# Optimization experiments

Hardware: AMD Instinct MI355X
Metric: run time of the kernel (lower is better)

## Reference

```python
import jax, jax.numpy as jnp
import numpy as np

EMBED_DIM = 2048
NUM_HEADS = 32
NUM_KV_HEADS = 8
HEAD_DIM = EMBED_DIM // NUM_HEADS  # 64
KV_DIM = HEAD_DIM * NUM_KV_HEADS   # 512
ROPE_BASE = 10000.0


def rope_cos_sin(seq_len, dim):
    inv_freq = 1.0 / (ROPE_BASE ** (jnp.arange(0, dim, 2, dtype=jnp.float32) / dim))
    t = jnp.arange(seq_len, dtype=jnp.float32)
    freqs = jnp.outer(t, inv_freq)                 # [T, dim/2]
    emb = jnp.concatenate([freqs, freqs], axis=-1)  # [T, dim]
    return jnp.cos(emb), jnp.sin(emb)


def rotate_half(x):
    half = x.shape[-1] // 2
    return jnp.concatenate([-x[..., half:], x[..., :half]], axis=-1)


def setup_inputs() -> dict:
    key = jax.random.key(0)
    k_x, k_q, k_k, k_v, k_o = jax.random.split(key, 5)
    B, T, C = 2, 2048, EMBED_DIM
    s = 1.0 / np.sqrt(C)
    x = jax.random.normal(k_x, (B, T, C), dtype=jnp.float32)
    # Linear weights stored as [in, out]; no bias (bias=False)
    Wq = jax.random.normal(k_q, (C, EMBED_DIM), dtype=jnp.float32) * s
    Wk = jax.random.normal(k_k, (C, KV_DIM), dtype=jnp.float32) * s
    Wv = jax.random.normal(k_v, (C, KV_DIM), dtype=jnp.float32) * s
    Wo = jax.random.normal(k_o, (C, EMBED_DIM), dtype=jnp.float32) * s
    return {"x": x, "Wq": Wq, "Wk": Wk, "Wv": Wv, "Wo": Wo}


def reference(x, Wq, Wk, Wv, Wo):
    B, T, C = x.shape
    H, KVH, D = NUM_HEADS, NUM_KV_HEADS, HEAD_DIM
    scale = D ** -0.5
    rep = H // KVH

    q = (x @ Wq).reshape(B, T, H, D).transpose(0, 2, 1, 3)    # [B,H,T,D]
    k = (x @ Wk).reshape(B, T, KVH, D).transpose(0, 2, 1, 3)  # [B,KVH,T,D]
    v = (x @ Wv).reshape(B, T, KVH, D).transpose(0, 2, 1, 3)
    # repeat_interleave over head dim to expand KV heads
    k = jnp.repeat(k, rep, axis=1)  # [B,H,T,D]
    v = jnp.repeat(v, rep, axis=1)

    cos, sin = rope_cos_sin(T, D)
    cos = cos[None, None, :, :]
    sin = sin[None, None, :, :]
    q = q * cos + rotate_half(q) * sin
    k = k * cos + rotate_half(k) * sin

    att = jnp.einsum('bhtd,bhsd->bhts', q, k) * scale  # [B,H,T,T]
    att = jax.nn.softmax(att, axis=-1)                 # mask=None, dropout eval
    y = jnp.einsum('bhts,bhsd->bhtd', att, v)          # [B,H,T,D]
    y = y.transpose(0, 2, 1, 3).reshape(B, T, C)
    return y @ Wo
```

## Files before the change

### kernel.cpp

```cpp
#include <hip/hip_runtime.h>
#include <stdint.h>

#define Tn   2048
#define Cn   2048
#define Hn   32
#define KVHn 8
#define Dn   64
#define MR   4096
#define NQKV 3072
#define KD   2048

typedef __attribute__((ext_vector_type(4))) float fx4;
typedef __attribute__((ext_vector_type(8))) short frag8;

#define MFMA(a,b,c) __builtin_amdgcn_mfma_f32_16x16x32_bf16((a),(b),(c),0,0,0)

struct __align__(16) U16x8 { unsigned short s[8]; };

__device__ __forceinline__ unsigned short f2bf(float x){
  union { float f; unsigned u; } v; v.f = x;
  return (unsigned short)((v.u + 0x7FFFu + ((v.u >> 16) & 1u)) >> 16);
}
__device__ __forceinline__ float bf2f(unsigned short h){
  union { unsigned u; float f; } v; v.u = ((unsigned)h) << 16; return v.f;
}
__device__ __forceinline__ float sexp2(float x){
#if __has_builtin(__builtin_amdgcn_exp2f)
  return __builtin_amdgcn_exp2f(x);
#else
  return exp2f(x);
#endif
}
__device__ __forceinline__ unsigned cvtpk(float a, float b){
  unsigned r; asm("v_cvt_pk_bf16_f32 %0, %1, %2" : "=v"(r) : "v"(a), "v"(b)); return r;
}

typedef const __attribute__((address_space(1))) void cas1_void;
typedef __attribute__((address_space(3))) void as3_void;
__device__ __forceinline__ void gld16(const void* g, void* l){
  __builtin_amdgcn_global_load_lds((cas1_void*)g, (as3_void*)l, 16, 0, 0);
}

__global__ __launch_bounds__(256) void k_prep(const float* __restrict__ x, unsigned short* __restrict__ xb,
                                              const float* __restrict__ Wq, const float* __restrict__ Wk,
                                              const float* __restrict__ Wv, unsigned short* __restrict__ wqkvt,
                                              const float* __restrict__ Wo, unsigned short* __restrict__ wot,
                                              float2* __restrict__ cs){
  __shared__ float tile[64][65];
  int blk = blockIdx.x, t = threadIdx.x;
  if (blk < 2048) {
    size_t blockbase = (size_t)blk * 4096;
    #pragma unroll
    for (int j = 0; j < 4; ++j) {
      size_t i = blockbase + j * 1024 + t * 4;
      float4 v = *(const float4*)(x + i);
      ushort4 o; o.x = f2bf(v.x); o.y = f2bf(v.y); o.z = f2bf(v.z); o.w = f2bf(v.w);
      *(ushort4*)(xb + i) = o;
    }
    return;
  }
  if (blk >= 4608) {
    int i = (blk - 4608) * 256 + t;
    int tp = i >> 5, d = i & 31;
    float inv = powf(10000.0f, -(float)d * (1.0f/32.0f));
    float fr = (float)tp * inv;
    cs[i] = make_float2(cosf(fr), sinf(fr));
    return;
  }
  const float* src; int col0, ld, n0, k0; unsigned short* outp;
  if (blk < 3584) {
    int bx = blk - 2048; n0 = (bx % 48) * 64; k0 = (bx / 48) * 64; outp = wqkvt;
    if (n0 < 2048)      { src = Wq; col0 = n0;        ld = 2048; }
    else if (n0 < 2560) { src = Wk; col0 = n0 - 2048; ld = 512;  }
    else                { src = Wv; col0 = n0 - 2560; ld = 512;  }
  } else {
    int bx = blk - 3584; n0 = (bx % 32) * 64; k0 = (bx / 32) * 64; outp = wot;
    src = Wo; col0 = n0; ld = 2048;
  }
  int r = t >> 2, cc = (t & 3) << 4;
  const float* p = src + (size_t)(k0 + r) * ld + col0 + cc;
  #pragma unroll
  for (int j = 0; j < 16; j += 4) {
    float4 v = *(const float4*)(p + j);
    tile[r][cc + j + 0] = v.x; tile[r][cc + j + 1] = v.y;
    tile[r][cc + j + 2] = v.z; tile[r][cc + j + 3] = v.w;
  }
  __syncthreads();
  int n = t >> 2, kc = (t & 3) << 4;
  unsigned short* q = outp + (size_t)(n0 + n) * 2048 + k0 + kc;
  U16x8 o0, o1;
  #pragma unroll
  for (int j = 0; j < 8; ++j) o0.s[j] = f2bf(tile[kc + j][n]);
  #pragma unroll
  for (int j = 0; j < 8; ++j) o1.s[j] = f2bf(tile[kc + 8 + j][n]);
  *(U16x8*)(q) = o0;
  *(U16x8*)(q + 8) = o1;
}

template<int MODE>
__global__ __launch_bounds__(256) void k_gemm(const unsigned short* __restrict__ A,
                                              const unsigned short* __restrict__ Bt,
                                              void* __restrict__ Cp,
                                              int M, int N, int K,
                                              const float2* __restrict__ cs){
  __shared__ unsigned short As[128 * 64];
  __shared__ unsigned short Bs[128 * 64];
  int tid = threadIdx.x;
  int m0 = blockIdx.y * 128, n0 = blockIdx.x * 128;
  int w = tid >> 6, ln = tid & 63, lr = ln & 15, lg = ln >> 4;
  int wm = (w >> 1) * 64, wn = (w & 1) * 64;
  fx4 acc[4][4];
  #pragma unroll
  for (int i = 0; i < 4; ++i)
    #pragma unroll
    for (int j = 0; j < 4; ++j) acc[i][j] = (fx4){0.f,0.f,0.f,0.f};
  int steps = K >> 6;
  for (int kt = 0; kt < steps; ++kt) {
    int kb = kt << 6;
    #pragma unroll
    for (int it = 0; it < 4; ++it) {
      int nch = it * 256 + tid;
      int r = nch >> 3, c = (nch & 7) ^ (r & 7);
      gld16(A  + (size_t)(m0 + r) * K + kb + c * 8, (char*)As + nch * 16);
      gld16(Bt + (size_t)(n0 + r) * K + kb + c * 8, (char*)Bs + nch * 16);
    }
    __syncthreads();
    frag8 aF[4][2], bF[4][2];
    #pragma unroll
    for (int i = 0; i < 4; ++i) {
      int ra = wm + i * 16 + lr;
      int rb = wn + i * 16 + lr;
      #pragma unroll
      for (int kk = 0; kk < 2; ++kk) {
        aF[i][kk] = *(const frag8*)((const char*)As + ra * 128 + (((lg + 4*kk) ^ (ra & 7)) << 4));
        bF[i][kk] = *(const frag8*)((const char*)Bs + rb * 128 + (((lg + 4*kk) ^ (rb & 7)) << 4));
      }
    }
    #pragma unroll
    for (int kk = 0; kk < 2; ++kk)
      #pragma unroll
      for (int i = 0; i < 4; ++i)
        #pragma unroll
        for (int j = 0; j < 4; ++j)
          acc[i][j] = MFMA(aF[i][kk], bF[j][kk], acc[i][j]);
    __syncthreads();
  }
  if (MODE == 0) {
    #pragma unroll
    for (int i = 0; i < 4; ++i) {
      int row = m0 + wm + i * 16 + lg * 4;
      #pragma unroll
      for (int j = 0; j < 4; ++j) {
        int col = n0 + wn + j * 16 + lr;
        #pragma unroll
        for (int rr = 0; rr < 4; ++rr)
          ((float*)Cp)[(size_t)(row + rr) * N + col] = acc[i][j][rr];
      }
    }
  } else {
    int nb = n0 + wn;
    unsigned short* outp = (unsigned short*)Cp;
    if (nb < 2560) {
      float sc = (n0 < 2048) ? 0.180336880f : 1.0f;
      #pragma unroll
      for (int i = 0; i < 4; ++i) {
        int rowb = m0 + wm + i * 16 + lg * 4;
        #pragma unroll
        for (int jp = 0; jp < 2; ++jp) {
          int dA = jp * 16 + lr;
          #pragma unroll
          for (int rr = 0; rr < 4; ++rr) {
            int row = rowb + rr;
            float2 cv = cs[((row & (Tn-1)) << 5) + dA];
            float a = acc[i][jp][rr], b = acc[i][jp + 2][rr];
            outp[(size_t)row * N + nb + dA]      = f2bf((a * cv.x - b * cv.y) * sc);
            outp[(size_t)row * N + nb + dA + 32] = f2bf((b * cv.x + a * cv.y) * sc);
          }
        }
      }
    } else {
      #pragma unroll
      for (int i = 0; i < 4; ++i) {
        int row = m0 + wm + i * 16 + lg * 4;
        #pragma unroll
        for (int j = 0; j < 4; ++j) {
          int col = nb + j * 16 + lr;
          #pragma unroll
          for (int rr = 0; rr < 4; ++rr)
            outp[(size_t)(row + rr) * N + col] = f2bf(acc[i][j][rr]);
        }
      }
    }
  }
}

__global__ __launch_bounds__(256) void k_vt(const unsigned short* __restrict__ qkv,
                                            unsigned short* __restrict__ vt){
  __shared__ unsigned short tl[64][66];
  int head = blockIdx.y;
  int b = head >> 3, kvh = head & 7;
  int t0 = blockIdx.x * 64;
  int t = threadIdx.x;
  int r = t >> 2, cc = (t & 3) << 4;
  const unsigned short* p = qkv + (size_t)(b * Tn + t0 + r) * NQKV + 2560 + kvh * 64 + cc;
  U16x8 v0 = *(const U16x8*)(p);
  U16x8 v1 = *(const U16x8*)(p + 8);
  #pragma unroll
  for (int j = 0; j < 8; ++j) { tl[r][cc + j] = v0.s[j]; tl[r][cc + 8 + j] = v1.s[j]; }
  __syncthreads();
  int d = t >> 2, cpair = t & 3;
  unsigned short* q = vt + ((size_t)head * 64 + d) * Tn + t0;
  #pragma unroll
  for (int ci = 0; ci < 2; ++ci) {
    int c = cpair * 2 + ci;
    U16x8 oo;
    #pragma unroll
    for (int e = 0; e < 8; ++e)
      oo.s[e] = tl[32 * (c >> 2) + 16 * (e >> 2) + 4 * (c & 3) + (e & 3)][d];
    *(U16x8*)(q + c * 8) = oo;
  }
}

__global__ __launch_bounds__(256) void k_attn(const unsigned short* __restrict__ qkv,
                                              const unsigned short* __restrict__ vt,
                                              unsigned short* __restrict__ y){
  __shared__ unsigned short Ks[2][64 * 64];
  __shared__ unsigned short Vs[2][64 * 64];
  int tid = threadIdx.x, w = tid >> 6, ln = tid & 63, lq = ln & 15, lg = ln >> 4;
  int bh = blockIdx.y, b = bh >> 5, h = bh & 31, kvh = h >> 2;
  int q0 = blockIdx.x * 128;
  frag8 qF[2][2];
  #pragma unroll
  for (int s = 0; s < 2; ++s) {
    const unsigned short* qrow = qkv + (size_t)(b * Tn + q0 + w * 32 + 16 * s + lq) * NQKV + h * 64;
    qF[s][0] = *(const frag8*)(qrow + lg * 8);
    qF[s][1] = *(const frag8*)(qrow + 32 + lg * 8);
  }
  fx4 zero4 = (fx4){0.f, 0.f, 0.f, 0.f};
  asm volatile("" : "+v"(zero4));
  int n0 = tid, n1 = 256 + tid;
  int r0 = n0 >> 3, c0 = (n0 & 7) ^ (r0 & 7);
  int r1 = n1 >> 3, c1 = (n1 & 7) ^ (r1 & 7);
  const unsigned short* kp0 = qkv + (size_t)b * Tn * NQKV + 2048 + kvh * 64 + (size_t)r0 * NQKV + c0 * 8;
  const unsigned short* kp1 = qkv + (size_t)b * Tn * NQKV + 2048 + kvh * 64 + (size_t)r1 * NQKV + c1 * 8;
  const unsigned short* vp0 = vt + ((size_t)(b * 8 + kvh) * 64 + r0) * Tn + c0 * 8;
  const unsigned short* vp1 = vt + ((size_t)(b * 8 + kvh) * 64 + r1) * Tn + c1 * 8;
  int koff0 = lq * 128 + (((lg)     ^ (lq & 7)) << 4);
  int koff1 = lq * 128 + (((lg + 4) ^ (lq & 7)) << 4);

#define STAGE(BUF) do {                                      \
    gld16(kp0, (char*)&Ks[BUF][0] + n0 * 16);                \
    gld16(kp1, (char*)&Ks[BUF][0] + n1 * 16);                \
    gld16(vp0, (char*)&Vs[BUF][0] + n0 * 16);                \
    gld16(vp1, (char*)&Vs[BUF][0] + n1 * 16);                \
    kp0 += 64 * NQKV; kp1 += 64 * NQKV; vp0 += 64; vp1 += 64;\
  } while (0)

#define PB(S, KK) ({ union { unsigned u[4]; frag8 f; } t_;                        \
    t_.u[0] = pu[S][2*(KK)][0]; t_.u[1] = pu[S][2*(KK)][1];                       \
    t_.u[2] = pu[S][2*(KK)+1][0]; t_.u[3] = pu[S][2*(KK)+1][1]; t_.f; })

#define PVSTEP do {                                                               \
    _Pragma("unroll")                                                             \
    for (int s = 0; s < 2; ++s)                                                   \
      _Pragma("unroll")                                                           \
      for (int df = 0; df < 4; ++df) {                                            \
        o[s][df] = MFMA(vf[df][0], PB(s, 0), o[s][df]);                           \
        o[s][df] = MFMA(vf[df][1], PB(s, 1), o[s][df]);                           \
      }                                                                           \
  } while (0)

#define TILE(BUF) do {                                                            \
    const char* kb_ = (const char*)&Ks[BUF][0];                                   \
    const char* vb_ = (const char*)&Vs[BUF][0];                                   \
    frag8 kf[4][2];                                                               \
    _Pragma("unroll")                                                             \
    for (int mf = 0; mf < 4; ++mf) {                                              \
      kf[mf][0] = *(const frag8*)(kb_ + mf * 2048 + koff0);                       \
      kf[mf][1] = *(const frag8*)(kb_ + mf * 2048 + koff1);                       \
    }                                                                             \
    __builtin_amdgcn_s_setprio(1);                                                \
    PVSTEP;                               \
    fx4 sf[2][4];                                                                 \
    _Pragma("unroll")                                                             \
    for (int s = 0; s < 2; ++s)                                                   \
      _Pragma("unroll")                                                           \
      for (int mf = 0; mf < 4; ++mf) {                                            \
        sf[s][mf] = MFMA(kf[mf][0], qF[s][0], zero4);                             \
        sf[s][mf] = MFMA(kf[mf][1], qF[s][1], sf[s][mf]);                         \
      }                                                                           \
    __builtin_amdgcn_s_setprio(0);                                                \
    _Pragma("unroll")              \
    for (int df = 0; df < 4; ++df) {                                              \
      vf[df][0] = *(const frag8*)(vb_ + df * 2048 + koff0);                       \
      vf[df][1] = *(const frag8*)(vb_ + df * 2048 + koff1);                       \
    }                                                                             \
    _Pragma("unroll")                                \
    for (int s = 0; s < 2; ++s) {                                                 \
      float ps = 0.f;                                                             \
      _Pragma("unroll")                                                           \
      for (int mf = 0; mf < 4; ++mf) {                                            \
        float p0 = sexp2(sf[s][mf][0]);                                           \
        float p1 = sexp2(sf[s][mf][1]);                                           \
        float p2 = sexp2(sf[s][mf][2]);                                           \
        float p3 = sexp2(sf[s][mf][3]);                                           \
        ps += (p0 + p1) + (p2 + p3);                                              \
        pu[s][mf][0] = cvtpk(p0, p1);                                             \
        pu[s][mf][1] = cvtpk(p2, p3);                                             \
      }                                                                           \
      lpart[s] += ps;                                                             \
    }                                                                             \
  } while (0)

  fx4 o[2][4];
  float lpart[2] = {0.f, 0.f};
  unsigned pu[2][4][2];
  frag8 vf[4][2];
  #pragma unroll
  for (int s = 0; s < 2; ++s) {
    #pragma unroll
    for (int i = 0; i < 4; ++i) o[s][i] = (fx4){0.f, 0.f, 0.f, 0.f};
    #pragma unroll
    for (int mf = 0; mf < 4; ++mf) { pu[s][mf][0] = 0u; pu[s][mf][1] = 0u; }
  }
  #pragma unroll
  for (int df = 0; df < 4; ++df) {
    vf[df][0] = (frag8){0,0,0,0,0,0,0,0};
    vf[df][1] = (frag8){0,0,0,0,0,0,0,0};
  }

  STAGE(0);
  __syncthreads();
  for (int kt = 0; kt < 32; kt += 2) {
    STAGE(1);
    TILE(0);
    __syncthreads();
    if (kt + 2 < 32) STAGE(0);
    TILE(1);
    __syncthreads();
  }
  __builtin_amdgcn_s_setprio(1);
  PVSTEP;
  __builtin_amdgcn_s_setprio(0);
#undef STAGE
#undef TILE
#undef PVSTEP
#undef PB

  #pragma unroll
  for (int s = 0; s < 2; ++s) {
    lpart[s] += __shfl_xor(lpart[s], 16);
    lpart[s] += __shfl_xor(lpart[s], 32);
    float inv = 1.0f / lpart[s];
    unsigned short* yp = y + (size_t)(b * Tn + q0 + w * 32 + 16 * s + lq) * Cn + h * 64;
    #pragma unroll
    for (int df = 0; df < 4; ++df) {
      unsigned lo = cvtpk(o[s][df][0] * inv, o[s][df][1] * inv);
      unsigned hi = cvtpk(o[s][df][2] * inv, o[s][df][3] * inv);
      *(uint2*)(yp + df * 16 + lg * 4) = make_uint2(lo, hi);
    }
  }
}

extern "C" void kernel_launch(void* const* d_in, const int* in_sizes, int n_in,
                              void* d_out, int out_size, void* d_ws, size_t ws_size,
                              hipStream_t stream){
  const float* x  = (const float*)d_in[0];
  const float* Wq = (const float*)d_in[1];
  const float* Wk = (const float*)d_in[2];
  const float* Wv = (const float*)d_in[3];
  const float* Wo = (const float*)d_in[4];
  char* ws = (char*)d_ws;
  size_t off = 0;
  unsigned short* xb    = (unsigned short*)(ws + off); off += (size_t)MR * KD * 2;
  unsigned short* wqkvt = (unsigned short*)(ws + off); off += (size_t)NQKV * KD * 2;
  unsigned short* wot   = (unsigned short*)(ws + off); off += (size_t)KD * KD * 2;
  unsigned short* qkv   = (unsigned short*)(ws + off); off += (size_t)MR * NQKV * 2;
  unsigned short* vtb   = (unsigned short*)(ws + off); off += (size_t)16 * 64 * Tn * 2;
  float2* cstab = (float2*)(ws + off); off += (size_t)Tn * 32 * 8;
  unsigned short* yb = xb;

  k_prep<<<4864, 256, 0, stream>>>(x, xb, Wq, Wk, Wv, wqkvt, Wo, wot, cstab);
  k_gemm<2><<<dim3(NQKV / 128, MR / 128), 256, 0, stream>>>(xb, wqkvt, qkv, MR, NQKV, KD, cstab);
  k_vt<<<dim3(Tn / 64, 16), 256, 0, stream>>>(qkv, vtb);
  k_attn<<<dim3(Tn / 128, 64), 256, 0, stream>>>(qkv, vtb, yb);
  k_gemm<0><<<dim3(KD / 128, MR / 128), 256, 0, stream>>>(yb, wot, d_out, MR, KD, KD, nullptr);
}
```

Baseline: 208.4 us.

## Grow attention blocks to 512 threads, double-buffer V fragments, swizzle GEMM grid

Attention blocks now cover 256 queries with 8 waves, so each staged K/V tile in shared memory serves twice as many queries and each thread issues half as many global-to-LDS loads. V fragments are read from LDS into alternating register sets at the start of each tile, so the PV step uses the previous tile's fragments and LDS reads overlap with MFMA work. The GEMM kernel remaps block indices with an XCD-style swizzle (stride by groups of 8) to improve L2 locality across the chiplets. The costs are more registers held per thread and fewer attention blocks, which could reduce occupancy.

New measurement: 208.7 us. Within noise of the previous version (+0.1%).

```diff
diff --git a/kernel.cpp b/kernel.cpp
--- a/kernel.cpp
+++ b/kernel.cpp
@@ -106,7 +106,11 @@
   __shared__ unsigned short As[128 * 64];
   __shared__ unsigned short Bs[128 * 64];
   int tid = threadIdx.x;
-  int m0 = blockIdx.y * 128, n0 = blockIdx.x * 128;
+  int nwg = gridDim.x * gridDim.y;
+  int lin = blockIdx.y * gridDim.x + blockIdx.x;
+  int swz = (lin & 7) * (nwg >> 3) + (lin >> 3);
+  int bx = swz % gridDim.x, by = swz / gridDim.x;
+  int m0 = by * 128, n0 = bx * 128;
   int w = tid >> 6, ln = tid & 63, lr = ln & 15, lg = ln >> 4;
   int wm = (w >> 1) * 64, wn = (w & 1) * 64;
   fx4 acc[4][4];
@@ -221,14 +225,14 @@
   }
 }
 
-__global__ __launch_bounds__(256) void k_attn(const unsigned short* __restrict__ qkv,
+__global__ __launch_bounds__(512) void k_attn(const unsigned short* __restrict__ qkv,
                                               const unsigned short* __restrict__ vt,
                                               unsigned short* __restrict__ y){
   __shared__ unsigned short Ks[2][64 * 64];
   __shared__ unsigned short Vs[2][64 * 64];
   int tid = threadIdx.x, w = tid >> 6, ln = tid & 63, lq = ln & 15, lg = ln >> 4;
   int bh = blockIdx.y, b = bh >> 5, h = bh & 31, kvh = h >> 2;
-  int q0 = blockIdx.x * 128;
+  int q0 = blockIdx.x * 256;
   frag8 qF[2][2];
   #pragma unroll
   for (int s = 0; s < 2; ++s) {
@@ -238,39 +242,34 @@
   }
   fx4 zero4 = (fx4){0.f, 0.f, 0.f, 0.f};
   asm volatile("" : "+v"(zero4));
-  int n0 = tid, n1 = 256 + tid;
+  int n0 = tid;
   int r0 = n0 >> 3, c0 = (n0 & 7) ^ (r0 & 7);
-  int r1 = n1 >> 3, c1 = (n1 & 7) ^ (r1 & 7);
   const unsigned short* kp0 = qkv + (size_t)b * Tn * NQKV + 2048 + kvh * 64 + (size_t)r0 * NQKV + c0 * 8;
-  const unsigned short* kp1 = qkv + (size_t)b * Tn * NQKV + 2048 + kvh * 64 + (size_t)r1 * NQKV + c1 * 8;
   const unsigned short* vp0 = vt + ((size_t)(b * 8 + kvh) * 64 + r0) * Tn + c0 * 8;
-  const unsigned short* vp1 = vt + ((size_t)(b * 8 + kvh) * 64 + r1) * Tn + c1 * 8;
   int koff0 = lq * 128 + (((lg)     ^ (lq & 7)) << 4);
   int koff1 = lq * 128 + (((lg + 4) ^ (lq & 7)) << 4);
 
 #define STAGE(BUF) do {                                      \
     gld16(kp0, (char*)&Ks[BUF][0] + n0 * 16);                \
-    gld16(kp1, (char*)&Ks[BUF][0] + n1 * 16);                \
     gld16(vp0, (char*)&Vs[BUF][0] + n0 * 16);                \
-    gld16(vp1, (char*)&Vs[BUF][0] + n1 * 16);                \
-    kp0 += 64 * NQKV; kp1 += 64 * NQKV; vp0 += 64; vp1 += 64;\
+    kp0 += 64 * NQKV; vp0 += 64;                             \
   } while (0)
 
 #define PB(S, KK) ({ union { unsigned u[4]; frag8 f; } t_;                        \
     t_.u[0] = pu[S][2*(KK)][0]; t_.u[1] = pu[S][2*(KK)][1];                       \
     t_.u[2] = pu[S][2*(KK)+1][0]; t_.u[3] = pu[S][2*(KK)+1][1]; t_.f; })
 
-#define PVSTEP do {                                                               \
+#define PVSTEP(VF) do {                                                           \
     _Pragma("unroll")                                                             \
     for (int s = 0; s < 2; ++s)                                                   \
       _Pragma("unroll")                                                           \
       for (int df = 0; df < 4; ++df) {                                            \
-        o[s][df] = MFMA(vf[df][0], PB(s, 0), o[s][df]);                           \
-        o[s][df] = MFMA(vf[df][1], PB(s, 1), o[s][df]);                           \
+        o[s][df] = MFMA(VF[df][0], PB(s, 0), o[s][df]);                           \
+        o[s][df] = MFMA(VF[df][1], PB(s, 1), o[s][df]);                           \
       }                                                                           \
   } while (0)
 
-#define TILE(BUF) do {                                                            \
+#define TILE(BUF, VFCUR, VFPREV) do {                                             \
     const char* kb_ = (const char*)&Ks[BUF][0];                                   \
     const char* vb_ = (const char*)&Vs[BUF][0];                                   \
     frag8 kf[4][2];                                                               \
@@ -279,8 +278,13 @@
       kf[mf][0] = *(const frag8*)(kb_ + mf * 2048 + koff0);                       \
       kf[mf][1] = *(const frag8*)(kb_ + mf * 2048 + koff1);                       \
     }                                                                             \
+    _Pragma("unroll")                                                             \
+    for (int df = 0; df < 4; ++df) {                                              \
+      VFCUR[df][0] = *(const frag8*)(vb_ + df * 2048 + koff0);                    \
+      VFCUR[df][1] = *(const frag8*)(vb_ + df * 2048 + koff1);                    \
+    }                                                                             \
     __builtin_amdgcn_s_setprio(1);                                                \
-    PVSTEP;                               \
+    PVSTEP(VFPREV);                       \
     fx4 sf[2][4];                                                                 \
     _Pragma("unroll")                                                             \
     for (int s = 0; s < 2; ++s)                                                   \
@@ -290,11 +294,6 @@
         sf[s][mf] = MFMA(kf[mf][1], qF[s][1], sf[s][mf]);                         \
       }                                                                           \
     __builtin_amdgcn_s_setprio(0);                                                \
-    _Pragma("unroll")              \
-    for (int df = 0; df < 4; ++df) {                                              \
-      vf[df][0] = *(const frag8*)(vb_ + df * 2048 + koff0);                       \
-      vf[df][1] = *(const frag8*)(vb_ + df * 2048 + koff1);                       \
-    }                                                                             \
     _Pragma("unroll")                                \
     for (int s = 0; s < 2; ++s) {                                                 \
       float ps = 0.f;                                                             \
@@ -315,7 +314,7 @@
   fx4 o[2][4];
   float lpart[2] = {0.f, 0.f};
   unsigned pu[2][4][2];
-  frag8 vf[4][2];
+  frag8 vfA[4][2], vfB[4][2];
   #pragma unroll
   for (int s = 0; s < 2; ++s) {
     #pragma unroll
@@ -325,22 +324,22 @@
   }
   #pragma unroll
   for (int df = 0; df < 4; ++df) {
-    vf[df][0] = (frag8){0,0,0,0,0,0,0,0};
-    vf[df][1] = (frag8){0,0,0,0,0,0,0,0};
+    vfA[df][0] = (frag8){0,0,0,0,0,0,0,0};
+    vfA[df][1] = (frag8){0,0,0,0,0,0,0,0};
   }
 
   STAGE(0);
   __syncthreads();
   for (int kt = 0; kt < 32; kt += 2) {
     STAGE(1);
-    TILE(0);
+    TILE(0, vfB, vfA);
     __syncthreads();
     if (kt + 2 < 32) STAGE(0);
-    TILE(1);
+    TILE(1, vfA, vfB);
     __syncthreads();
   }
   __builtin_amdgcn_s_setprio(1);
-  PVSTEP;
+  PVSTEP(vfA);
   __builtin_amdgcn_s_setprio(0);
 #undef STAGE
 #undef TILE
@@ -383,6 +382,6 @@
   k_prep<<<4864, 256, 0, stream>>>(x, xb, Wq, Wk, Wv, wqkvt, Wo, wot, cstab);
   k_gemm<2><<<dim3(NQKV / 128, MR / 128), 256, 0, stream>>>(xb, wqkvt, qkv, MR, NQKV, KD, cstab);
   k_vt<<<dim3(Tn / 64, 16), 256, 0, stream>>>(qkv, vtb);
-  k_attn<<<dim3(Tn / 128, 64), 256, 0, stream>>>(qkv, vtb, yb);
+  k_attn<<<dim3(Tn / 256, 64), 512, 0, stream>>>(qkv, vtb, yb);
   k_gemm<0><<<dim3(KD / 128, MR / 128), 256, 0, stream>>>(yb, wot, d_out, MR, KD, KD, nullptr);
 }
```
